# Performance work log

Hardware: AMD Instinct MI355X
Metric: run time of the kernel (lower is better)

The kernel has to match this reference:

```python
import jax, jax.numpy as jnp
import numpy as np

NUM_CLASSES = 1203
NO_OBJECT_WEIGHT = 0.1


def setup_inputs() -> dict:
    key = jax.random.key(0)
    k1, k2, k3, k4 = jax.random.split(key, 4)
    B, Q, T = 64, 1024, 32
    pred_logits = jax.random.normal(k1, (B, Q, NUM_CLASSES + 1), dtype=jnp.float32)
    pred_boxes = jax.random.uniform(k2, (B, Q, 4), dtype=jnp.float32)
    tgt_labels = jax.random.randint(k3, (B, T), 0, NUM_CLASSES)
    tgt_boxes = jax.random.uniform(k4, (B, T, 4), dtype=jnp.float32)
    return {"pred_logits": pred_logits, "pred_boxes": pred_boxes,
            "tgt_labels": tgt_labels, "tgt_boxes": tgt_boxes}


def _lsa(cost):
    """Rectangular linear sum assignment (Jonker-Volgenant shortest augmenting
    path, same algorithm as scipy.optimize.linear_sum_assignment)."""
    cost = np.asarray(cost, dtype=np.float64)
    transposed = cost.shape[0] > cost.shape[1]
    if transposed:
        cost = cost.T
    n, m = cost.shape
    u = np.zeros(n)
    v = np.zeros(m)
    path = np.full(m, -1, dtype=np.int64)
    col4row = np.full(n, -1, dtype=np.int64)
    row4col = np.full(m, -1, dtype=np.int64)
    for cur_row in range(n):
        shortest = np.full(m, np.inf)
        SR = np.zeros(n, dtype=bool)
        SC = np.zeros(m, dtype=bool)
        min_val = 0.0
        i = cur_row
        sink = -1
        while sink == -1:
            SR[i] = True
            rem = np.nonzero(~SC)[0]
            r = min_val + cost[i, rem] - u[i] - v[rem]
            upd = r < shortest[rem]
            shortest[rem[upd]] = r[upd]
            path[rem[upd]] = i
            j = rem[np.argmin(shortest[rem])]
            min_val = shortest[j]
            SC[j] = True
            if row4col[j] == -1:
                sink = j
            else:
                i = row4col[j]
        u[cur_row] += min_val
        other = SR.copy()
        other[cur_row] = False
        u[other] += min_val - shortest[col4row[other]]
        v[SC] -= min_val - shortest[SC]
        j = sink
        while True:
            i = path[j]
            row4col[j] = i
            col4row[i], j = j, col4row[i]
            if i == cur_row:
                break
    if transposed:
        order = np.argsort(col4row)
        return col4row[order], order
    return np.arange(n), col4row


def _match(pred_logits, pred_boxes, tgt_labels, tgt_boxes):
    """Hungarian matching on detached costs (host-side, like the original
    .detach().cpu() + scipy loop). Returns src (query) / col (target) indices
    of shape [B, T]."""
    probs = np.asarray(jax.nn.softmax(pred_logits, axis=-1))
    pb = np.asarray(pred_boxes)
    tb = np.asarray(tgt_boxes)
    labels = np.asarray(tgt_labels)
    B, Q, _ = probs.shape
    T = labels.shape[1]
    # cost_class[b,q,t] = -probs[b,q,labels[b,t]]
    cost_class = -probs[np.arange(B)[:, None, None],
                        np.arange(Q)[None, :, None],
                        labels[:, None, :]]
    # cost_bbox[b,q,t] = L1 distance between pred box q and tgt box t
    cost_bbox = np.abs(pb[:, :, None, :] - tb[:, None, :, :]).sum(-1)
    C = cost_bbox + cost_class
    src = np.zeros((B, T), dtype=np.int64)
    col = np.zeros((B, T), dtype=np.int64)
    for b in range(B):
        r, c = _lsa(C[b])
        src[b], col[b] = r, c
    return src, col


def reference(pred_logits, pred_boxes, tgt_labels, tgt_boxes):
    src_np, col_np = _match(pred_logits, pred_boxes, tgt_labels, tgt_boxes)
    src = jnp.asarray(src_np)   # [B, T] matched query indices
    col = jnp.asarray(col_np)   # [B, T] matched target indices
    labels = jnp.asarray(tgt_labels)
    B, Q, Cp1 = pred_logits.shape
    bidx = jnp.arange(B)[:, None]

    matched_labels = jnp.take_along_axis(labels, col, axis=1)  # [B, T]
    target_classes = jnp.full((B, Q), NUM_CLASSES, dtype=jnp.int32)
    target_classes = target_classes.at[bidx, src].set(matched_labels.astype(jnp.int32))

    # weighted cross-entropy (weight[no_object] = NO_OBJECT_WEIGHT, mean = sum(w*nll)/sum(w))
    weight = jnp.ones(Cp1, dtype=jnp.float32).at[NUM_CLASSES].set(NO_OBJECT_WEIGHT)
    logp = jax.nn.log_softmax(pred_logits, axis=-1)
    nll = -jnp.take_along_axis(logp, target_classes[..., None], axis=-1)[..., 0]
    wt = weight[target_classes]
    loss_ce = jnp.sum(wt * nll) / jnp.sum(wt)

    matched_pred = pred_boxes[bidx, src]                              # [B, T, 4]
    matched_tgt = jnp.take_along_axis(tgt_boxes, col[:, :, None], axis=1)  # [B, T, 4]
    loss_bbox = jnp.mean(jnp.abs(matched_pred - matched_tgt))

    return loss_ce + 5.0 * loss_bbox
```

## Files before the change

kernel.cpp:

```cpp
#include <hip/hip_runtime.h>
#include <math.h>

#define NCLS 1203
#define CP1 1204
#define BB 64
#define QQ 1024
#define TT 32
#define NO_OBJ_W 0.1

__device__ inline double shfl_xor_dbl(double x, int mask) {
    long long v = __double_as_longlong(x);
    int lo = (int)(v & 0xffffffffLL);
    int hi = (int)((unsigned long long)v >> 32);
    lo = __shfl_xor(lo, mask);
    hi = __shfl_xor(hi, mask);
    return __longlong_as_double(((long long)hi << 32) | (unsigned long long)(unsigned int)lo);
}
__device__ inline unsigned long long shfl_xor_u64(unsigned long long x, int mask) {
    int lo = __shfl_xor((int)(x & 0xffffffffull), mask);
    int hi = __shfl_xor((int)(x >> 32), mask);
    return ((unsigned long long)(unsigned)hi << 32) | (unsigned)lo;
}
__device__ inline unsigned fkey(float f) {
    unsigned b = __float_as_uint(f);
    return (b & 0x80000000u) ? ~b : (b | 0x80000000u);
}
__device__ inline float funkey(unsigned k) {
    return __uint_as_float((k & 0x80000000u) ? (k & 0x7fffffffu) : ~k);
}

__global__ __launch_bounds__(256) void k_stats_cost(
    const float* __restrict__ logits, const float* __restrict__ pboxes,
    const int* __restrict__ labels, const float* __restrict__ tboxes,
    float* __restrict__ stats, double* __restrict__ partials,
    float* __restrict__ costQ, unsigned long long* __restrict__ pmin,
    int* __restrict__ done)
{
    __shared__ __align__(16) float lds_row[4][CP1];
    __shared__ unsigned long long kmin[4][TT];
    __shared__ double pwave[4];
    __shared__ float Lv[4];

    int tid = threadIdx.x;
    int w = tid >> 6, lane = tid & 63;
    int b = blockIdx.x >> 8;
    int q0 = (blockIdx.x & 255) << 2;
    int rowid = (b << 10) + q0 + w;

    if (blockIdx.x == 0 && tid == 0) *done = 0;

    int lab_r = 0;
    float4 tb4 = make_float4(0.f, 0.f, 0.f, 0.f);
    if (lane < TT) {
        lab_r = labels[b * TT + lane];
        tb4 = ((const float4*)tboxes)[b * TT + lane];
    }
    float4 pb = ((const float4*)pboxes)[rowid];

    const float4* r4 = (const float4*)(logits + (size_t)rowid * CP1);
    float4 cx0 = r4[lane];
    float4 cx1 = r4[lane + 64];
    float4 cx2 = r4[lane + 128];
    float4 cx3 = r4[lane + 192];
    float4 cx4 = (lane < 45) ? r4[lane + 256]
                             : make_float4(-INFINITY, -INFINITY, -INFINITY, -INFINITY);

    float4* Lr4 = (float4*)lds_row[w];
    Lr4[lane] = cx0;
    Lr4[lane + 64] = cx1;
    Lr4[lane + 128] = cx2;
    Lr4[lane + 192] = cx3;
    if (lane < 45) Lr4[lane + 256] = cx4;

    float s = __expf(cx0.x) + __expf(cx0.y) + __expf(cx0.z) + __expf(cx0.w);
    s += __expf(cx1.x) + __expf(cx1.y) + __expf(cx1.z) + __expf(cx1.w);
    s += __expf(cx2.x) + __expf(cx2.y) + __expf(cx2.z) + __expf(cx2.w);
    s += __expf(cx3.x) + __expf(cx3.y) + __expf(cx3.z) + __expf(cx3.w);
    if (lane < 45)
        s += __expf(cx4.x) + __expf(cx4.y) + __expf(cx4.z) + __expf(cx4.w);
    #pragma unroll
    for (int off = 32; off; off >>= 1) s += __shfl_xor(s, off);

    float L = __logf(s);
    float lno = __shfl(cx4.w, 44);

    if (lane == 0) {
        Lv[w] = L;
        pwave[w] = 0.1 * ((double)L - (double)lno);
    }

    if (lane < TT) {
        float lg = lds_row[w][lab_r];
        float prob = __expf(lg - L);
        float bbx = fabsf(pb.x - tb4.x) + fabsf(pb.y - tb4.y)
                  + fabsf(pb.z - tb4.z) + fabsf(pb.w - tb4.w);
        float cst = bbx - prob;
        costQ[(size_t)rowid * TT + lane] = cst;
        kmin[w][lane] = ((unsigned long long)fkey(cst) << 32) | (unsigned)(q0 + w);
    }
    __syncthreads();
    if (tid == 0) {
        partials[blockIdx.x] = pwave[0] + pwave[1] + pwave[2] + pwave[3];
        *(float4*)(stats + (b << 10) + q0) = make_float4(Lv[0], Lv[1], Lv[2], Lv[3]);
    }
    if (tid < TT) {
        unsigned long long k0 = kmin[0][tid];
        unsigned long long k1 = kmin[1][tid];
        unsigned long long k2 = kmin[2][tid];
        unsigned long long k3 = kmin[3][tid];
        if (k1 < k0) k0 = k1;
        if (k2 < k0) k0 = k2;
        if (k3 < k0) k0 = k3;
        pmin[(size_t)blockIdx.x * TT + tid] = k0;
    }
}

__global__ __launch_bounds__(1024) void k_hungarian(
    const float* __restrict__ costQ, const float* __restrict__ logits,
    const float* __restrict__ pboxes, const float* __restrict__ tboxes,
    const int* __restrict__ labels, const float* __restrict__ stats,
    const double* __restrict__ partials, const unsigned long long* __restrict__ pmin,
    double* __restrict__ triples, int* __restrict__ done, float* __restrict__ out)
{
    __shared__ float ldsC[TT][QQ + 1];
    __shared__ unsigned long long kcomb[1024];
    __shared__ float sh_lds[QQ];
    __shared__ int path_lds[QQ];
    __shared__ int r4c_lds[QQ];
    __shared__ unsigned long long key_lds[TT];
    __shared__ int c4r_lds[TT];
    __shared__ float u_lds[TT];
    __shared__ int flag_lds;

    int b = blockIdx.x;
    int tid = threadIdx.x;
    int w = tid >> 6, lane = tid & 63;
    const float* C = costQ + (size_t)b * QQ * TT;

    r4c_lds[tid] = -1;
    {
        int t0 = tid & 31, c = tid >> 5;
        unsigned long long key = ~0ull;
        #pragma unroll
        for (int j = 0; j < 8; ++j) {
            unsigned long long kk = pmin[((size_t)b * 256 + c * 8 + j) * TT + t0];
            if (kk < key) key = kk;
        }
        kcomb[tid] = key;
    }
    __syncthreads();

    unsigned long long um = 0;
    int myc = -1;
    if (w == 0) {
        if (lane < TT) {
            unsigned long long key = ~0ull;
            #pragma unroll
            for (int c = 0; c < 32; ++c) {
                unsigned long long kk = kcomb[c * 32 + lane];
                if (kk < key) key = kk;
            }
            key_lds[lane] = key;
        }
        for (int i = 0; i < TT; ++i) {
            unsigned long long key = key_lds[i];
            int jmin = (int)(unsigned)(key & 0xffffffffull);
            if (lane == i) u_lds[i] = funkey((unsigned)(key >> 32));
            unsigned long long taken = __ballot(myc == jmin);
            if (!taken && lane == i) myc = jmin;
        }
        if (lane < TT) c4r_lds[lane] = myc;
        if (lane < TT && myc >= 0) r4c_lds[myc] = lane;
        um = __ballot(lane < TT && myc < 0);
        if (lane == 0) flag_lds = (um != 0ull) ? 1 : 0;
    }
    __syncthreads();

    if (flag_lds) {
        const float4* C4 = (const float4*)C;
        #pragma unroll
        for (int it = 0; it < 8; ++it) {
            int idx4 = it * 1024 + tid;
            float4 v = C4[idx4];
            int q = idx4 >> 3;
            int tq = (idx4 & 7) << 2;
            ldsC[tq][q] = v.x;
            ldsC[tq + 1][q] = v.y;
            ldsC[tq + 2][q] = v.z;
            ldsC[tq + 3][q] = v.w;
        }
        __syncthreads();
    }
    if (w != 0) return;

    float v_reg[16];
    #pragma unroll
    for (int k = 0; k < 16; ++k) v_reg[k] = 0.0f;
    float sh_reg[16];
    while (um) {
        int cur = __ffsll(um) - 1;
        um &= um - 1;
        #pragma unroll
        for (int k = 0; k < 16; ++k) sh_reg[k] = INFINITY;
        unsigned SC = 0;
        unsigned SRm = 0;
        float minVal = 0.0f;
        int i = cur;
        int sink = -1;

        while (sink < 0) {
            SRm |= 1u << i;
            float ui = u_lds[i];
            float ci[16];
            #pragma unroll
            for (int k = 0; k < 16; ++k) ci[k] = ldsC[i][k * 64 + lane];
            #pragma unroll
            for (int k = 0; k < 16; ++k) {
                if (!((SC >> k) & 1)) {
                    float r = minVal + ci[k] - ui - v_reg[k];
                    if (r < sh_reg[k]) {
                        sh_reg[k] = r;
                        int j = k * 64 + lane;
                        sh_lds[j] = r;
                        path_lds[j] = i;
                    }
                }
            }
            unsigned long long key = ~0ull;
            #pragma unroll
            for (int k = 0; k < 16; ++k) {
                if (!((SC >> k) & 1)) {
                    unsigned long long kk = ((unsigned long long)fkey(sh_reg[k]) << 32) | (unsigned)(k * 64 + lane);
                    if (kk < key) key = kk;
                }
            }
            #pragma unroll
            for (int off = 32; off; off >>= 1) {
                unsigned long long o = shfl_xor_u64(key, off);
                if (o < key) key = o;
            }
            minVal = funkey((unsigned)(key >> 32));
            int jstar = (int)(unsigned)(key & 0xffffffffull);
            if (lane == (jstar & 63)) SC |= 1u << (jstar >> 6);
            int rj = r4c_lds[jstar];
            if (rj < 0) sink = jstar; else i = rj;
        }

        if (lane == 0) u_lds[cur] += minVal;
        if (lane < TT && lane != cur && ((SRm >> lane) & 1))
            u_lds[lane] += minVal - sh_lds[c4r_lds[lane]];
        #pragma unroll
        for (int k = 0; k < 16; ++k)
            if ((SC >> k) & 1) v_reg[k] -= (minVal - sh_reg[k]);
        if (lane == 0) {
            int j = sink;
            while (true) {
                int ii = path_lds[j];
                r4c_lds[j] = ii;
                int nj = c4r_lds[ii];
                c4r_lds[ii] = j;
                j = nj;
                if (ii == cur) break;
            }
        }
    }

    double wn = 0.0;
    {
        const double* pp = partials + (size_t)b * 256;
        #pragma unroll
        for (int r = 0; r < 4; ++r) wn += pp[lane * 4 + r];
    }
    double bbox = 0.0;
    if (lane < TT) {
        int qv = c4r_lds[lane];
        int rid = (b << 10) + qv;
        int lb = labels[b * TT + lane];
        double L = (double)stats[rid];
        double lg = (double)logits[(size_t)rid * CP1 + lb];
        double lno = (double)logits[(size_t)rid * CP1 + NCLS];
        wn += (L - lg) - 0.1 * (L - lno);
        float4 p4 = ((const float4*)pboxes)[rid];
        float4 t4 = ((const float4*)tboxes)[b * TT + lane];
        bbox = fabs((double)p4.x - (double)t4.x) + fabs((double)p4.y - (double)t4.y)
             + fabs((double)p4.z - (double)t4.z) + fabs((double)p4.w - (double)t4.w);
    }
    #pragma unroll
    for (int off = 32; off; off >>= 1) {
        wn += shfl_xor_dbl(wn, off);
        bbox += shfl_xor_dbl(bbox, off);
    }
    if (lane == 0) { triples[b * 2] = wn; triples[b * 2 + 1] = bbox; }

    int old = 0;
    if (lane == 0) {
        __threadfence();
        old = atomicAdd(done, 1);
    }
    old = __shfl(old, 0);
    if (old == BB - 1) {
        __threadfence();
        double a = triples[lane * 2];
        double bx = triples[lane * 2 + 1];
        #pragma unroll
        for (int off = 32; off; off >>= 1) {
            a += shfl_xor_dbl(a, off);
            bx += shfl_xor_dbl(bx, off);
        }
        if (lane == 0) {
            double wt = NO_OBJ_W * (double)(BB * QQ - BB * TT) + (double)(BB * TT);
            out[0] = (float)(a / wt + 5.0 * (bx / (double)(BB * TT * 4)));
        }
    }
}

extern "C" void kernel_launch(void* const* d_in, const int* in_sizes, int n_in,
                              void* d_out, int out_size, void* d_ws, size_t ws_size,
                              hipStream_t stream) {
    const float* logits = (const float*)d_in[0];
    const float* pboxes = (const float*)d_in[1];
    const int*   labels = (const int*)d_in[2];
    const float* tboxes = (const float*)d_in[3];
    float* out = (float*)d_out;

    char* ws = (char*)d_ws;
    float*  costQ    = (float*)ws;
    float*  stats    = (float*)(ws + 8388608);
    unsigned long long* pmin = (unsigned long long*)(ws + 8650752);
    double* partials = (double*)(ws + 12845056);
    double* triples  = (double*)(ws + 12976128);
    int*    done     = (int*)(ws + 12977152);

    hipLaunchKernelGGL(k_stats_cost, dim3(BB * 256), dim3(256), 0, stream,
                       logits, pboxes, labels, tboxes, stats, partials,
                       costQ, pmin, done);
    hipLaunchKernelGGL(k_hungarian, dim3(BB), dim3(1024), 0, stream,
                       costQ, logits, pboxes, tboxes, labels, stats, partials,
                       pmin, triples, done, out);
}
```

Before: 74.82 us.

## Drop LDS cost staging in Hungarian kernel; read cost directly from global

The Hungarian kernel no longer transposes the per-batch 32x1024 cost matrix into shared memory. Each augmenting step now reads cost entries straight from global memory with a stride of 32 floats. The block shrinks from 1024 to 256 threads, and each thread reduces 32 pmin partials instead of 8. This removes the 128KB LDS staging and its block-wide sync, but the uncoalesced global reads sit on the serial augmenting-path critical loop whenever the greedy initial assignment leaves rows unmatched.

Measured after the change: 77.90 us. 4.1% more time.

```diff
diff --git a/kernel.cpp b/kernel.cpp
--- a/kernel.cpp
+++ b/kernel.cpp
@@ -28,6 +28,7 @@
 __device__ inline float funkey(unsigned k) {
     return __uint_as_float((k & 0x80000000u) ? (k & 0x7fffffffu) : ~k);
 }
+
 
 __global__ __launch_bounds__(256) void k_stats_cost(
     const float* __restrict__ logits, const float* __restrict__ pboxes,
@@ -115,84 +116,66 @@
     }
 }
 
-__global__ __launch_bounds__(1024) void k_hungarian(
+__global__ __launch_bounds__(256) void k_hungarian(
     const float* __restrict__ costQ, const float* __restrict__ logits,
     const float* __restrict__ pboxes, const float* __restrict__ tboxes,
     const int* __restrict__ labels, const float* __restrict__ stats,
     const double* __restrict__ partials, const unsigned long long* __restrict__ pmin,
     double* __restrict__ triples, int* __restrict__ done, float* __restrict__ out)
 {
-    __shared__ float ldsC[TT][QQ + 1];
-    __shared__ unsigned long long kcomb[1024];
+    __shared__ unsigned long long kcomb[256];
     __shared__ float sh_lds[QQ];
     __shared__ int path_lds[QQ];
     __shared__ int r4c_lds[QQ];
-    __shared__ unsigned long long key_lds[TT];
-    __shared__ int c4r_lds[TT];
-    __shared__ float u_lds[TT];
-    __shared__ int flag_lds;
+    __shared__ unsigned long long key_l[TT];
+    __shared__ int c4r_l[TT];
+    __shared__ float u_l[TT];
 
     int b = blockIdx.x;
     int tid = threadIdx.x;
     int w = tid >> 6, lane = tid & 63;
-    const float* C = costQ + (size_t)b * QQ * TT;
 
     r4c_lds[tid] = -1;
+    r4c_lds[tid + 256] = -1;
+    r4c_lds[tid + 512] = -1;
+    r4c_lds[tid + 768] = -1;
     {
         int t0 = tid & 31, c = tid >> 5;
         unsigned long long key = ~0ull;
-        #pragma unroll
-        for (int j = 0; j < 8; ++j) {
-            unsigned long long kk = pmin[((size_t)b * 256 + c * 8 + j) * TT + t0];
+        const unsigned long long* pm = pmin + (size_t)b * 256 * TT;
+        #pragma unroll
+        for (int j = 0; j < 32; ++j) {
+            unsigned long long kk = pm[(size_t)((c << 5) + j) * TT + t0];
             if (kk < key) key = kk;
         }
         kcomb[tid] = key;
     }
     __syncthreads();
+    if (w != 0) return;
 
     unsigned long long um = 0;
     int myc = -1;
-    if (w == 0) {
-        if (lane < TT) {
-            unsigned long long key = ~0ull;
-            #pragma unroll
-            for (int c = 0; c < 32; ++c) {
-                unsigned long long kk = kcomb[c * 32 + lane];
-                if (kk < key) key = kk;
-            }
-            key_lds[lane] = key;
-        }
-        for (int i = 0; i < TT; ++i) {
-            unsigned long long key = key_lds[i];
-            int jmin = (int)(unsigned)(key & 0xffffffffull);
-            if (lane == i) u_lds[i] = funkey((unsigned)(key >> 32));
-            unsigned long long taken = __ballot(myc == jmin);
-            if (!taken && lane == i) myc = jmin;
-        }
-        if (lane < TT) c4r_lds[lane] = myc;
-        if (lane < TT && myc >= 0) r4c_lds[myc] = lane;
-        um = __ballot(lane < TT && myc < 0);
-        if (lane == 0) flag_lds = (um != 0ull) ? 1 : 0;
-    }
-    __syncthreads();
-
-    if (flag_lds) {
-        const float4* C4 = (const float4*)C;
-        #pragma unroll
-        for (int it = 0; it < 8; ++it) {
-            int idx4 = it * 1024 + tid;
-            float4 v = C4[idx4];
-            int q = idx4 >> 3;
-            int tq = (idx4 & 7) << 2;
-            ldsC[tq][q] = v.x;
-            ldsC[tq + 1][q] = v.y;
-            ldsC[tq + 2][q] = v.z;
-            ldsC[tq + 3][q] = v.w;
-        }
-        __syncthreads();
-    }
-    if (w != 0) return;
-
+    if (lane < TT) {
+        unsigned long long key = ~0ull;
+        #pragma unroll
+        for (int c = 0; c < 8; ++c) {
+            unsigned long long kk = kcomb[c * 32 + lane];
+            if (kk < key) key = kk;
+        }
+        key_l[lane] = key;
+    }
+    for (int i = 0; i < TT; ++i) {
+        unsigned long long key = key_l[i];
+        int jmin = (int)(unsigned)(key & 0xffffffffull);
+        if (lane == i) u_l[i] = funkey((unsigned)(key >> 32));
+        unsigned long long taken = __ballot(myc == jmin);
+        if (!taken && lane == i) myc = jmin;
+    }
+    if (lane < TT) c4r_l[lane] = myc;
+    if (lane < TT && myc >= 0) r4c_lds[myc] = lane;
+    um = __ballot(lane < TT && myc < 0);
+
+    const float* Cb = costQ + (size_t)b * QQ * TT;
     float v_reg[16];
     #pragma unroll
     for (int k = 0; k < 16; ++k) v_reg[k] = 0.0f;
@@ -210,10 +193,10 @@
 
         while (sink < 0) {
             SRm |= 1u << i;
-            float ui = u_lds[i];
+            float ui = u_l[i];
             float ci[16];
             #pragma unroll
-            for (int k = 0; k < 16; ++k) ci[k] = ldsC[i][k * 64 + lane];
+            for (int k = 0; k < 16; ++k) ci[k] = Cb[(size_t)(k * 64 + lane) * TT + i];
             #pragma unroll
             for (int k = 0; k < 16; ++k) {
                 if (!((SC >> k) & 1)) {
@@ -246,9 +229,9 @@
             if (rj < 0) sink = jstar; else i = rj;
         }
 
-        if (lane == 0) u_lds[cur] += minVal;
+        if (lane == 0) u_l[cur] += minVal;
         if (lane < TT && lane != cur && ((SRm >> lane) & 1))
-            u_lds[lane] += minVal - sh_lds[c4r_lds[lane]];
+            u_l[lane] += minVal - sh_lds[c4r_l[lane]];
         #pragma unroll
         for (int k = 0; k < 16; ++k)
             if ((SC >> k) & 1) v_reg[k] -= (minVal - sh_reg[k]);
@@ -257,8 +240,8 @@
             while (true) {
                 int ii = path_lds[j];
                 r4c_lds[j] = ii;
-                int nj = c4r_lds[ii];
-                c4r_lds[ii] = j;
+                int nj = c4r_l[ii];
+                c4r_l[ii] = j;
                 j = nj;
                 if (ii == cur) break;
             }
@@ -273,7 +256,7 @@
     }
     double bbox = 0.0;
     if (lane < TT) {
-        int qv = c4r_lds[lane];
+        int qv = c4r_l[lane];
         int rid = (b << 10) + qv;
         int lb = labels[b * TT + lane];
         double L = (double)stats[rid];
@@ -334,7 +317,7 @@
     hipLaunchKernelGGL(k_stats_cost, dim3(BB * 256), dim3(256), 0, stream,
                        logits, pboxes, labels, tboxes, stats, partials,
                        costQ, pmin, done);
-    hipLaunchKernelGGL(k_hungarian, dim3(BB), dim3(1024), 0, stream,
+    hipLaunchKernelGGL(k_hungarian, dim3(BB), dim3(256), 0, stream,
                        costQ, logits, pboxes, tboxes, labels, stats, partials,
                        pmin, triples, done, out);
 }
```
